# Kernel optimization log

Measured on AMD Instinct MI355X. Metric: run time of the kernel, lower is better.

The kernel has to match this reference:

```python
import jax, jax.numpy as jnp
import numpy as np

N = 8192      # nodes (= hidden_channels / heads)
E = 262144    # edges (avg degree 32)
IN = 256      # in_channels
H = 8         # heads
C = 32        # out_channels per head
NEG_SLOPE = 0.2


def setup_inputs() -> dict:
    key = jax.random.key(0)
    ks = jax.random.split(key, 8)
    x = jax.random.normal(ks[0], (N, IN), jnp.float32)
    edge_index = jax.random.randint(ks[1], (2, E), 0, N, dtype=jnp.int32)
    lin_w = jax.random.normal(ks[2], (H * C, IN), jnp.float32) * (1.0 / np.sqrt(IN))
    att_src = jax.random.normal(ks[3], (H, C), jnp.float32) * 0.1
    att_dst = jax.random.normal(ks[4], (H, C), jnp.float32) * 0.1
    bias = jax.random.normal(ks[5], (H * C,), jnp.float32) * 0.01
    out_w = jax.random.normal(ks[6], (C, N * H * C), jnp.float32) * (1.0 / np.sqrt(N * H * C))
    out_b = jax.random.normal(ks[7], (C,), jnp.float32) * 0.01
    return {"x": x, "edge_index": edge_index, "lin_w": lin_w, "att_src": att_src,
            "att_dst": att_dst, "bias": bias, "out_w": out_w, "out_b": out_b}


def reference(x, edge_index, lin_w, att_src, att_dst, bias, out_w, out_b):
    n = x.shape[0]
    # PyG GATConv default: add self loops
    loop = jnp.arange(n, dtype=edge_index.dtype)
    src = jnp.concatenate([edge_index[0], loop])  # message sources j
    dst = jnp.concatenate([edge_index[1], loop])  # message targets i
    # per-head linear projection: [n, H, C]
    xh = (x @ lin_w.T).reshape(n, H, C)
    a_src = jnp.einsum('nhc,hc->nh', xh, att_src)  # [n, H]
    a_dst = jnp.einsum('nhc,hc->nh', xh, att_dst)  # [n, H]
    # edge attention logits + segment softmax over incoming edges of each dst
    e = jax.nn.leaky_relu(a_src[src] + a_dst[dst], negative_slope=NEG_SLOPE)  # [E', H]
    m = jax.ops.segment_max(e, dst, num_segments=n)        # [n, H]
    ex = jnp.exp(e - m[dst])
    denom = jax.ops.segment_sum(ex, dst, num_segments=n)   # [n, H]
    alpha = ex / denom[dst]                                 # [E', H]
    # weighted scatter-add aggregation
    agg = jax.ops.segment_sum(alpha[:, :, None] * xh[src], dst, num_segments=n)  # [n, H, C]
    out = agg.reshape(n, H * C) + bias
    # flatten all nodes, dense output layer, softmax
    y = out.reshape(-1) @ out_w.T + out_b  # [C]
    return jax.nn.softmax(y)
```

## Files before the change

### kernel.cpp

```cpp
#include <hip/hip_runtime.h>


namespace {
constexpr int  kN    = 8192;
constexpr int  kE    = 262144;
constexpr int  kTotE = kE + kN;
constexpr long kK    = 2097152;
constexpr int  kNCH  = 64;
}

typedef float vfloat4 __attribute__((ext_vector_type(4)));

static __device__ __forceinline__ ushort f2bf(float f) {
  unsigned u = __float_as_uint(f);
  return (ushort)((u + 0x7FFFu + ((u >> 16) & 1u)) >> 16);
}
static __device__ __forceinline__ float bf2f(ushort b) {
  return __uint_as_float(((unsigned)b) << 16);
}

__global__ __launch_bounds__(256) void gemm_xh(const float* __restrict__ x,
                                               const float* __restrict__ lw,
                                               float* __restrict__ xh,
                                               ushort* __restrict__ xh_bf) {
  __shared__ float As[16][68];
  __shared__ float Bs[16][68];
  const int t  = threadIdx.x;
  const int tx = t & 15, ty = t >> 4;
  const int rowBase = blockIdx.x * 64;
  const int colBase = blockIdx.y * 64;
  const int lr = t >> 2;
  const int lk = (t & 3) * 4;

  float acc[4][4] = {};
  for (int kc = 0; kc < 256; kc += 16) {
    float4 av = *(const float4*)(x  + (long)(rowBase + lr) * 256 + kc + lk);
    float4 bv = *(const float4*)(lw + (long)(colBase + lr) * 256 + kc + lk);
    __syncthreads();
    As[lk + 0][lr] = av.x; As[lk + 1][lr] = av.y; As[lk + 2][lr] = av.z; As[lk + 3][lr] = av.w;
    Bs[lk + 0][lr] = bv.x; Bs[lk + 1][lr] = bv.y; Bs[lk + 2][lr] = bv.z; Bs[lk + 3][lr] = bv.w;
    __syncthreads();
#pragma unroll
    for (int k = 0; k < 16; k++) {
      float4 a4 = *(const float4*)(&As[k][ty * 4]);
      float4 b4 = *(const float4*)(&Bs[k][tx * 4]);
      float aa[4] = {a4.x, a4.y, a4.z, a4.w};
      float bb[4] = {b4.x, b4.y, b4.z, b4.w};
#pragma unroll
      for (int i = 0; i < 4; i++)
#pragma unroll
        for (int j = 0; j < 4; j++) acc[i][j] += aa[i] * bb[j];
    }
  }
#pragma unroll
  for (int i = 0; i < 4; i++) {
    const long row = rowBase + ty * 4 + i;
    float4 o = make_float4(acc[i][0], acc[i][1], acc[i][2], acc[i][3]);
    *(float4*)(xh + row * 256 + colBase + tx * 4) = o;
    ushort4 ob = make_ushort4(f2bf(o.x), f2bf(o.y), f2bf(o.z), f2bf(o.w));
    *(ushort4*)(xh_bf + row * 256 + colBase + tx * 4) = ob;
  }
}

__global__ __launch_bounds__(256) void att_deg(const float* __restrict__ xh,
                                               const float* __restrict__ att_s,
                                               const float* __restrict__ att_d,
                                               const int* __restrict__ ei,
                                               float* __restrict__ a_src,
                                               float* __restrict__ a_dst,
                                               int* __restrict__ cnt) {
  const int n = blockIdx.x, t = threadIdx.x;
  float v = xh[(long)n * 256 + t];
  float s = v * att_s[t];
  float d = v * att_d[t];
#pragma unroll
  for (int off = 16; off; off >>= 1) {
    s += __shfl_down(s, off, 32);
    d += __shfl_down(d, off, 32);
  }
  if ((t & 31) == 0) {
    a_src[n * 8 + (t >> 5)] = s;
    a_dst[n * 8 + (t >> 5)] = d;
  }
  const int gid = n * 256 + t;
  if (gid < kE) atomicAdd(&cnt[ei[kE + gid]], 1);
}

__global__ __launch_bounds__(1024) void scan_cnt(const int* __restrict__ cnt,
                                                 int* __restrict__ rowptr,
                                                 int* __restrict__ wpos) {
  __shared__ int s[1024];
  const int t = threadIdx.x;
  int v[8]; int sum = 0;
#pragma unroll
  for (int q = 0; q < 8; q++) { v[q] = cnt[t * 8 + q] + 1; sum += v[q]; }
  s[t] = sum;
  __syncthreads();
  for (int off = 1; off < 1024; off <<= 1) {
    int add = (t >= off) ? s[t - off] : 0;
    __syncthreads();
    s[t] += add;
    __syncthreads();
  }
  int excl = s[t] - sum;
#pragma unroll
  for (int q = 0; q < 8; q++) {
    rowptr[t * 8 + q] = excl;
    wpos[t * 8 + q]   = excl;
    excl += v[q];
  }
  if (t == 1023) rowptr[kN] = s[1023];
}

__global__ __launch_bounds__(256) void scatter_csr(const int* __restrict__ ei,
                                                   const float* __restrict__ a_src,
                                                   const float* __restrict__ a_dst,
                                                   int* __restrict__ wpos,
                                                   int* __restrict__ csr,
                                                   float* __restrict__ w8) {
  int idx = blockIdx.x * 256 + threadIdx.x;
  if (idx >= kTotE) return;
  int s, d;
  if (idx < kE) { s = ei[idx]; d = ei[kE + idx]; }
  else          { s = idx - kE; d = s; }
  int pos = atomicAdd(&wpos[d], 1);
  csr[pos] = s;
  float4 s0 = *(const float4*)(a_src + s * 8);
  float4 s1 = *(const float4*)(a_src + s * 8 + 4);
  float4 d0 = *(const float4*)(a_dst + d * 8);
  float4 d1 = *(const float4*)(a_dst + d * 8 + 4);
  float e[8] = {s0.x + d0.x, s0.y + d0.y, s0.z + d0.z, s0.w + d0.w,
                s1.x + d1.x, s1.y + d1.y, s1.z + d1.z, s1.w + d1.w};
  float w[8];
#pragma unroll
  for (int h = 0; h < 8; h++) {
    float ee = (e[h] > 0.f) ? e[h] : 0.2f * e[h];
    w[h] = __expf(ee);
  }
  float4* wp = (float4*)(w8 + (long)pos * 8);
  wp[0] = make_float4(w[0], w[1], w[2], w[3]);
  wp[1] = make_float4(w[4], w[5], w[6], w[7]);
}

__global__ __launch_bounds__(256) void agg_kernel(const ushort* __restrict__ xb,
                                                  const float* __restrict__ w8,
                                                  const int* __restrict__ rowptr,
                                                  const int* __restrict__ csr,
                                                  const float* __restrict__ bias,
                                                  float* __restrict__ out_flat) {
  const int i = blockIdx.x, t = threadIdx.x, h = t >> 5;
  const int beg = rowptr[i], end = rowptr[i + 1];
  float acc = 0.f, den = 0.f;
  int j = beg;
  for (; j + 8 <= end; j += 8) {
    int   s[8]; float w[8]; float f[8];
#pragma unroll
    for (int q = 0; q < 8; q++) s[q] = csr[j + q];
#pragma unroll
    for (int q = 0; q < 8; q++) w[q] = w8[(long)(j + q) * 8 + h];
#pragma unroll
    for (int q = 0; q < 8; q++) f[q] = bf2f(xb[(long)s[q] * 256 + t]);
#pragma unroll
    for (int q = 0; q < 8; q++) { den += w[q]; acc += w[q] * f[q]; }
  }
  for (; j < end; j++) {
    int s0 = csr[j];
    float w0 = w8[(long)j * 8 + h];
    den += w0;
    acc += w0 * bf2f(xb[(long)s0 * 256 + t]);
  }
  out_flat[(long)i * 256 + t] = acc / den + bias[t];
}

__global__ __launch_bounds__(256) void final_dot(const float* __restrict__ of,
                                                 const float* __restrict__ w,
                                                 float* __restrict__ part) {
  const int t = threadIdx.x, b = blockIdx.x;
  const int c = b >> 6;
  const long k0 = (long)(b & 63) * 32768;
  const float* __restrict__ wr = w + (long)c * kK + k0;
  const float* __restrict__ fr = of + k0;
  float acc = 0.f;
#pragma unroll 8
  for (int i = 0; i < 32; i++) {
    const int k = i * 1024 + t * 4;
    vfloat4 wv = __builtin_nontemporal_load((const vfloat4*)(wr + k));
    float4  f  = *(const float4*)(fr + k);
    acc += wv.x * f.x + wv.y * f.y + wv.z * f.z + wv.w * f.w;
  }
  acc += __shfl_down(acc, 32, 64);
  acc += __shfl_down(acc, 16, 64);
  acc += __shfl_down(acc, 8, 64);
  acc += __shfl_down(acc, 4, 64);
  acc += __shfl_down(acc, 2, 64);
  acc += __shfl_down(acc, 1, 64);
  __shared__ float s4[4];
  const int lane = t & 63, wid = t >> 6;
  if (lane == 0) s4[wid] = acc;
  __syncthreads();
  if (t == 0) part[(b & 63) * 32 + c] = s4[0] + s4[1] + s4[2] + s4[3];
}

__global__ __launch_bounds__(1024) void finalize(const float* __restrict__ part,
                                                 const float* __restrict__ ob,
                                                 float* __restrict__ out) {
  __shared__ float s[32][33];
  const int t = threadIdx.x;
  const int c = t & 31, r = t >> 5;
  float sum = 0.f;
  for (int i = r; i < kNCH; i += 32) sum += part[i * 32 + c];
  s[c][r] = sum;
  __syncthreads();
  if (t < 32) {
    float y = ob[t];
#pragma unroll
    for (int r2 = 0; r2 < 32; r2++) y += s[t][r2];
    float m = y;
#pragma unroll
    for (int off = 16; off; off >>= 1) m = fmaxf(m, __shfl_xor(m, off, 32));
    float e = __expf(y - m);
    float d = e;
#pragma unroll
    for (int off = 16; off; off >>= 1) d += __shfl_xor(d, off, 32);
    out[t] = e / d;
  }
}

extern "C" void kernel_launch(void* const* d_in, const int* in_sizes, int n_in,
                              void* d_out, int out_size, void* d_ws, size_t ws_size,
                              hipStream_t stream) {
  (void)in_sizes; (void)n_in; (void)out_size; (void)ws_size;
  const float* x     = (const float*)d_in[0];
  const int*   ei    = (const int*)  d_in[1];
  const float* lin_w = (const float*)d_in[2];
  const float* att_s = (const float*)d_in[3];
  const float* att_d = (const float*)d_in[4];
  const float* bias  = (const float*)d_in[5];
  const float* out_w = (const float*)d_in[6];
  const float* out_b = (const float*)d_in[7];
  float* out = (float*)d_out;

  float*  xh       = (float*)d_ws;
  float*  out_flat = xh + kK;
  float*  a_src    = out_flat + kK;
  float*  a_dst    = a_src + kN * 8;
  float*  part     = a_dst + kN * 8;
  float*  w8       = part + (long)kNCH * 32;
  ushort* xh_bf    = (ushort*)(w8 + (long)kTotE * 8);
  int*    cnt      = (int*)(xh_bf + kK);
  int*    rowptr   = cnt + kN;
  int*    wpos     = rowptr + (kN + 1);
  int*    csr      = wpos + kN;

  (void)hipMemsetAsync(cnt, 0, kN * sizeof(int), stream);
  gemm_xh    <<<dim3(128, 4), 256, 0, stream>>>(x, lin_w, xh, xh_bf);
  att_deg    <<<kN, 256, 0, stream>>>(xh, att_s, att_d, ei, a_src, a_dst, cnt);
  scan_cnt   <<<1, 1024, 0, stream>>>(cnt, rowptr, wpos);
  scatter_csr<<<(kTotE + 255) / 256, 256, 0, stream>>>(ei, a_src, a_dst, wpos, csr, w8);
  agg_kernel <<<kN, 256, 0, stream>>>(xh_bf, w8, rowptr, csr, bias, out_flat);
  final_dot  <<<32 * kNCH, 256, 0, stream>>>(out_flat, out_w, part);
  finalize   <<<1, 1024, 0, stream>>>(part, out_b, out);
}
```

Before: 432.5 us.

## Fuse final dense dot product into aggregation kernel with atomic partial sums

The aggregation kernel now also computes each node's contribution to the 32 output logits. It prefetches that node's slice of out_w with nontemporal loads before the gather loop, then reduces the products through wavefronts and atomically adds them into 256 partial-sum buckets. This drops the separate final_dot kernel and the write and re-read of the full out_flat buffer. In exchange it adds register pressure from holding 8 vfloat4 weights per thread, plus atomic contention and nondeterministic float summation order.

```diff
diff --git a/kernel.cpp b/kernel.cpp
--- a/kernel.cpp
+++ b/kernel.cpp
@@ -6,7 +6,7 @@
 constexpr int  kE    = 262144;
 constexpr int  kTotE = kE + kN;
 constexpr long kK    = 2097152;
-constexpr int  kNCH  = 64;
+constexpr int  kYB   = 256;
 }
 
 typedef float vfloat4 __attribute__((ext_vector_type(4)));
@@ -142,26 +142,37 @@
   wp[1] = make_float4(w[4], w[5], w[6], w[7]);
 }
 
-__global__ __launch_bounds__(256) void agg_kernel(const ushort* __restrict__ xb,
-                                                  const float* __restrict__ w8,
-                                                  const int* __restrict__ rowptr,
-                                                  const int* __restrict__ csr,
-                                                  const float* __restrict__ bias,
-                                                  float* __restrict__ out_flat) {
+__global__ __launch_bounds__(256) void agg_dot(const ushort* __restrict__ xb,
+                                               const float* __restrict__ w8,
+                                               const int* __restrict__ rowptr,
+                                               const int* __restrict__ csr,
+                                               const float* __restrict__ bias,
+                                               const float* __restrict__ w,
+                                               float* __restrict__ ypart) {
   const int i = blockIdx.x, t = threadIdx.x, h = t >> 5;
+  const int lane = t & 63, wid = t >> 6;
+
+  const long wbase = (long)i * 256 + lane * 4;
+  vfloat4 wv[8];
+#pragma unroll
+  for (int cc = 0; cc < 8; cc++) {
+    const int c = cc * 4 + wid;
+    wv[cc] = __builtin_nontemporal_load((const vfloat4*)(w + (long)c * kK + wbase));
+  }
+
   const int beg = rowptr[i], end = rowptr[i + 1];
   float acc = 0.f, den = 0.f;
   int j = beg;
   for (; j + 8 <= end; j += 8) {
-    int   s[8]; float w[8]; float f[8];
+    int   s[8]; float ww[8]; float f[8];
 #pragma unroll
     for (int q = 0; q < 8; q++) s[q] = csr[j + q];
 #pragma unroll
-    for (int q = 0; q < 8; q++) w[q] = w8[(long)(j + q) * 8 + h];
+    for (int q = 0; q < 8; q++) ww[q] = w8[(long)(j + q) * 8 + h];
 #pragma unroll
     for (int q = 0; q < 8; q++) f[q] = bf2f(xb[(long)s[q] * 256 + t]);
 #pragma unroll
-    for (int q = 0; q < 8; q++) { den += w[q]; acc += w[q] * f[q]; }
+    for (int q = 0; q < 8; q++) { den += ww[q]; acc += ww[q] * f[q]; }
   }
   for (; j < end; j++) {
     int s0 = csr[j];
@@ -169,46 +180,35 @@
     den += w0;
     acc += w0 * bf2f(xb[(long)s0 * 256 + t]);
   }
-  out_flat[(long)i * 256 + t] = acc / den + bias[t];
-}
-
-__global__ __launch_bounds__(256) void final_dot(const float* __restrict__ of,
-                                                 const float* __restrict__ w,
-                                                 float* __restrict__ part) {
-  const int t = threadIdx.x, b = blockIdx.x;
-  const int c = b >> 6;
-  const long k0 = (long)(b & 63) * 32768;
-  const float* __restrict__ wr = w + (long)c * kK + k0;
-  const float* __restrict__ fr = of + k0;
-  float acc = 0.f;
-#pragma unroll 8
-  for (int i = 0; i < 32; i++) {
-    const int k = i * 1024 + t * 4;
-    vfloat4 wv = __builtin_nontemporal_load((const vfloat4*)(wr + k));
-    float4  f  = *(const float4*)(fr + k);
-    acc += wv.x * f.x + wv.y * f.y + wv.z * f.z + wv.w * f.w;
-  }
-  acc += __shfl_down(acc, 32, 64);
-  acc += __shfl_down(acc, 16, 64);
-  acc += __shfl_down(acc, 8, 64);
-  acc += __shfl_down(acc, 4, 64);
-  acc += __shfl_down(acc, 2, 64);
-  acc += __shfl_down(acc, 1, 64);
-  __shared__ float s4[4];
-  const int lane = t & 63, wid = t >> 6;
-  if (lane == 0) s4[wid] = acc;
-  __syncthreads();
-  if (t == 0) part[(b & 63) * 32 + c] = s4[0] + s4[1] + s4[2] + s4[3];
-}
-
-__global__ __launch_bounds__(1024) void finalize(const float* __restrict__ part,
+
+  __shared__ float ofs[256];
+  __shared__ float yb[32];
+  ofs[t] = acc / den + bias[t];
+  __syncthreads();
+  float4 f4 = *(const float4*)(ofs + lane * 4);
+#pragma unroll
+  for (int cc = 0; cc < 8; cc++) {
+    float p = wv[cc].x * f4.x + wv[cc].y * f4.y + wv[cc].z * f4.z + wv[cc].w * f4.w;
+    p += __shfl_down(p, 32, 64);
+    p += __shfl_down(p, 16, 64);
+    p += __shfl_down(p, 8, 64);
+    p += __shfl_down(p, 4, 64);
+    p += __shfl_down(p, 2, 64);
+    p += __shfl_down(p, 1, 64);
+    if (lane == 0) yb[cc * 4 + wid] = p;
+  }
+  __syncthreads();
+  if (t < 32) atomicAdd(&ypart[(i & (kYB - 1)) * 32 + t], yb[t]);
+}
+
+__global__ __launch_bounds__(1024) void finalize(const float* __restrict__ ypart,
                                                  const float* __restrict__ ob,
                                                  float* __restrict__ out) {
   __shared__ float s[32][33];
   const int t = threadIdx.x;
   const int c = t & 31, r = t >> 5;
   float sum = 0.f;
-  for (int i = r; i < kNCH; i += 32) sum += part[i * 32 + c];
+  for (int q = r; q < kYB; q += 32) sum += ypart[q * 32 + c];
   s[c][r] = sum;
   __syncthreads();
   if (t < 32) {
@@ -241,23 +241,21 @@
   float* out = (float*)d_out;
 
   float*  xh       = (float*)d_ws;
-  float*  out_flat = xh + kK;
-  float*  a_src    = out_flat + kK;
+  float*  a_src    = xh + kK;
   float*  a_dst    = a_src + kN * 8;
-  float*  part     = a_dst + kN * 8;
-  float*  w8       = part + (long)kNCH * 32;
+  float*  w8       = a_dst + kN * 8;
   ushort* xh_bf    = (ushort*)(w8 + (long)kTotE * 8);
   int*    cnt      = (int*)(xh_bf + kK);
-  int*    rowptr   = cnt + kN;
+  float*  ypart    = (float*)(cnt + kN);
+  int*    rowptr   = (int*)(ypart + kYB * 32);
   int*    wpos     = rowptr + (kN + 1);
   int*    csr      = wpos + kN;
 
-  (void)hipMemsetAsync(cnt, 0, kN * sizeof(int), stream);
+  (void)hipMemsetAsync(cnt, 0, kN * sizeof(int) + kYB * 32 * sizeof(float), stream);
   gemm_xh    <<<dim3(128, 4), 256, 0, stream>>>(x, lin_w, xh, xh_bf);
   att_deg    <<<kN, 256, 0, stream>>>(xh, att_s, att_d, ei, a_src, a_dst, cnt);
   scan_cnt   <<<1, 1024, 0, stream>>>(cnt, rowptr, wpos);
   scatter_csr<<<(kTotE + 255) / 256, 256, 0, stream>>>(ei, a_src, a_dst, wpos, csr, w8);
-  agg_kernel <<<kN, 256, 0, stream>>>(xh_bf, w8, rowptr, csr, bias, out_flat);
-  final_dot  <<<32 * kNCH, 256, 0, stream>>>(out_flat, out_w, part);
-  finalize   <<<1, 1024, 0, stream>>>(part, out_b, out);
-}
+  agg_dot    <<<kN, 256, 0, stream>>>(xh_bf, w8, rowptr, csr, bias, out_w, ypart);
+  finalize   <<<1, 1024, 0, stream>>>(ypart, out_b, out);
+}
```

Result: no change. 432.6 us (+0.0%).
